# Optimization experiments

Hardware: AMD Instinct MI355X
Metric: run time of the kernel (lower is better)

The kernel has to match this reference:

```python
import jax, jax.numpy as jnp
import numpy as np

BATCH = 256
NUM_PIXELS = 4096
NUM_LATENT = 8192
NUM_STEPS = 50
STEP_SIZE = 0.1
SPARSE_MULT = 0.1
EPS = 1e-8


def setup_inputs() -> dict:
    key = jax.random.key(0)
    k1, k2 = jax.random.split(key)
    input_tensor = jax.random.normal(k1, (BATCH, NUM_PIXELS), dtype=jnp.float32)
    w = jax.random.normal(k2, (NUM_PIXELS, NUM_LATENT), dtype=jnp.float32)
    # l2-normalize each dictionary element (column over pixel dim), as in dp.l2_normalize_weights
    w = w / (jnp.linalg.norm(w, axis=0, keepdims=True) + EPS)
    return {"input_tensor": input_tensor, "w": w}


def _threshold(u):
    # soft threshold with rectify_a=True: a = max(u - lambda, 0)
    return jnp.where(u > SPARSE_MULT, u - SPARSE_MULT, jnp.zeros_like(u))


def reference(input_tensor, w):
    # excitatory drive b = x @ w, constant over inference steps  [B, L]
    excitatory = jnp.matmul(input_tensor, w)
    # inhibitory Gram matrix G = w^T w - I  [L, L]
    gram = jnp.matmul(w.T, w) - jnp.eye(NUM_LATENT, dtype=w.dtype)

    def body(u, _):
        a = _threshold(u)
        du = excitatory - jnp.matmul(a, gram) - u
        return u + STEP_SIZE * du, None

    u0 = jnp.zeros((input_tensor.shape[0], NUM_LATENT), dtype=input_tensor.dtype)
    u_final, _ = jax.lax.scan(body, u0, None, length=NUM_STEPS - 1)
    a_final = _threshold(u_final)
    # reconstruction = a @ w^T  [B, P]
    return jnp.matmul(a_final, w.T)
```

## Files before the change

kernel.cpp:

```cpp
#include <hip/hip_runtime.h>
#include <stdint.h>
#include <math.h>

#define B_DIM 256
#define P_DIM 4096
#define L_DIM 8192
#define NSTEPS 50
#define STEP 0.1f
#define LAM 0.1f
#define FP8_ITERS 42
#define GSCALE 64.0f
#define ASCALE 16.0f
#define INV_SCALE (1.0f / (64.0f * 16.0f))

typedef __attribute__((ext_vector_type(8))) short bf16x8;
typedef __attribute__((ext_vector_type(4))) float f32x4;
typedef __attribute__((ext_vector_type(4))) int i32x4;
typedef __attribute__((ext_vector_type(8))) int i32x8;

__device__ __forceinline__ unsigned short f2bf(float f) {
    union { float f; uint32_t u; } x; x.f = f;
    uint32_t r = (x.u + 0x7FFF + ((x.u >> 16) & 1)) >> 16;
    return (unsigned short)r;
}
__device__ __forceinline__ float bf2f(unsigned short h) {
    union { uint32_t u; float f; } x; x.u = (uint32_t)h << 16; return x.f;
}


__global__ void cast_x_kernel(const float* __restrict__ in, unsigned short* __restrict__ out, int n) {
    int i = (blockIdx.x * blockDim.x + threadIdx.x) * 4;
    if (i < n) {
        float4 v = *(const float4*)&in[i];
        ushort4 o;
        o.x = f2bf(v.x); o.y = f2bf(v.y); o.z = f2bf(v.z); o.w = f2bf(v.w);
        *(ushort4*)&out[i] = o;
    }
}

__global__ void cast_transpose_w(const float* __restrict__ w,
                                 unsigned short* __restrict__ w_bf,
                                 unsigned short* __restrict__ wT_bf) {
    __shared__ float tile[32][33];
    int c0 = blockIdx.x * 32;
    int r0 = blockIdx.y * 32;
    int tx = threadIdx.x, ty = threadIdx.y;
#pragma unroll
    for (int i = ty; i < 32; i += 8) {
        float v = w[(size_t)(r0 + i) * L_DIM + c0 + tx];
        tile[i][tx] = v;
        w_bf[(size_t)(r0 + i) * L_DIM + c0 + tx] = f2bf(v);
    }
    __syncthreads();
#pragma unroll
    for (int i = ty; i < 32; i += 8) {
        wT_bf[(size_t)(c0 + i) * P_DIM + r0 + tx] = f2bf(tile[tx][i]);
    }
}

__global__ void quantize_G(const unsigned short* __restrict__ G, unsigned char* __restrict__ Gf) {
    size_t i = ((size_t)blockIdx.x * 256 + threadIdx.x) * 8;
    bf16x8 v = *(const bf16x8*)&G[i];
    float f[8];
#pragma unroll
    for (int j = 0; j < 8; ++j) f[j] = bf2f((unsigned short)v[j]) * GSCALE;
    int q0 = __builtin_amdgcn_cvt_pk_fp8_f32(f[0], f[1], 0, false);
    q0 = __builtin_amdgcn_cvt_pk_fp8_f32(f[2], f[3], q0, true);
    int q1 = __builtin_amdgcn_cvt_pk_fp8_f32(f[4], f[5], 0, false);
    q1 = __builtin_amdgcn_cvt_pk_fp8_f32(f[6], f[7], q1, true);
    const int r = (int)(i & 127);
    size_t dst = (i & ~(size_t)127) + (size_t)((((r >> 6) & 1) << 6) + (((r >> 3) & 3) << 4) + (((r >> 5) & 1) << 3));
    *(int2*)(Gf + dst) = make_int2(q0, q1);
}

template <int BM, int BN, int BK, int WMC, int WNC, int EPI, int MM, int NN, int KK, int MAP>
__global__ __launch_bounds__(WMC * WNC * 64)
void gemm_pipe(const unsigned short* __restrict__ A,
               const unsigned short* __restrict__ Bt,
               float* __restrict__ Cf,
               float* __restrict__ uvec,
               unsigned short* __restrict__ aout,
               unsigned char* __restrict__ afp8) {
    constexpr int NWAVES = WMC * WNC;
    constexpr int WM = BM / WMC, WN = BN / WNC;
    constexpr int MF = WM / 16, NF = WN / 16;
    constexpr int ACH = BM / (8 * NWAVES);
    constexpr int BCH = BN / (8 * NWAVES);
    constexpr int LPS = ACH + BCH;
    constexpr int NT = KK / BK;
    static_assert(BK == 64, "swizzle hardcoded for BK=64");
    static_assert(ACH * 8 * NWAVES == BM && BCH * 8 * NWAVES == BN, "stage geometry");
    static_assert(NT % 4 == 0 && NT >= 8, "pipeline geometry");

    __shared__ __align__(16) unsigned short As[4][BM * BK];
    __shared__ __align__(16) unsigned short Bs[4][BN * BK];

    const int tid = threadIdx.x;
    const int w = tid >> 6;
    const int l = tid & 63;
    const int wr = w / WNC, wc = w % WNC;

    const int id = blockIdx.x;
    int bx, by;
    if constexpr (MAP == 0) {
        constexpr int PPX = (NN / BN) / 8;
        static_assert(MM / BM == 4 && (NN / BN) % 8 == 0, "panel map geometry");
        bx = (id & 7) * PPX + ((id >> 3) >> 2);
        by = (id >> 3) & 3;
    } else {
        constexpr int GY = MM / BM;
        by = id % GY;
        bx = id / GY;
    }
    const int row0 = by * BM;
    const int col0 = bx * BN;

    const int lrow = l >> 3;
    const int lcol = (((l & 7) ^ lrow) * 8);

    const unsigned short* gA = A + (size_t)(row0 + lrow) * KK + lcol;
    const unsigned short* gB = Bt + (size_t)(col0 + lrow) * KK + lcol;

    auto stage = [&](int buf, int k0) {
#pragma unroll
        for (int i = 0; i < ACH; ++i) {
            const int chunk = i * NWAVES + w;
            __builtin_amdgcn_global_load_lds(
                (const __attribute__((address_space(1))) void*)(gA + (size_t)chunk * 8 * KK + k0),
                (__attribute__((address_space(3))) void*)(&As[buf][chunk * 512]), 16, 0, 0);
        }
#pragma unroll
        for (int i = 0; i < BCH; ++i) {
            const int chunk = i * NWAVES + w;
            __builtin_amdgcn_global_load_lds(
                (const __attribute__((address_space(1))) void*)(gB + (size_t)chunk * 8 * KK + k0),
                (__attribute__((address_space(3))) void*)(&Bs[buf][chunk * 512]), 16, 0, 0);
        }
    };

    f32x4 acc[MF][NF] = {};

    auto compute = [&](int buf) {
#pragma unroll
        for (int kk = 0; kk < BK; kk += 32) {
            const int kslot = (kk >> 3) + (l >> 4);
            bf16x8 af[MF], bfr[NF];
#pragma unroll
            for (int mf = 0; mf < MF; ++mf) {
                const int arow = wr * WM + mf * 16 + (l & 15);
                af[mf] = *(const bf16x8*)&As[buf][arow * BK + ((kslot ^ (arow & 7)) << 3)];
            }
#pragma unroll
            for (int nf = 0; nf < NF; ++nf) {
                const int brow = wc * WN + nf * 16 + (l & 15);
                bfr[nf] = *(const bf16x8*)&Bs[buf][brow * BK + ((kslot ^ (brow & 7)) << 3)];
            }
#pragma unroll
            for (int mf = 0; mf < MF; ++mf)
#pragma unroll
                for (int nf = 0; nf < NF; ++nf)
                    acc[mf][nf] = __builtin_amdgcn_mfma_f32_16x16x32_bf16(
                        af[mf], bfr[nf], acc[mf][nf], 0, 0, 0);
        }
    };

#define PH(BUF, TT, WAITN, DOSTG)                                            \
    asm volatile("s_waitcnt vmcnt(%0)" ::"i"(WAITN) : "memory");             \
    __builtin_amdgcn_s_barrier();                                            \
    asm volatile("" ::: "memory");                                           \
    if (DOSTG) stage((BUF + 3) & 3, ((TT) + 3) * BK);                        \
    compute(BUF);

    stage(0, 0);
    stage(1, BK);
    stage(2, 2 * BK);
#pragma unroll 1
    for (int t = 0; t < NT - 4; t += 4) {
        PH(0, t + 0, 2 * LPS, true)
        PH(1, t + 1, 2 * LPS, true)
        PH(2, t + 2, 2 * LPS, true)
        PH(3, t + 3, 2 * LPS, true)
    }
    PH(0, NT - 4, 2 * LPS, true)
    PH(1, NT - 3, 2 * LPS, false)
    PH(2, NT - 2, LPS, false)
    PH(3, NT - 1, 0, false)
#undef PH

    const int er = (l >> 4) * 4;
    const int ec = l & 15;
#pragma unroll
    for (int mf = 0; mf < MF; ++mf) {
#pragma unroll
        for (int nf = 0; nf < NF; ++nf) {
#pragma unroll
            for (int j = 0; j < 4; ++j) {
                int gr = row0 + wr * WM + mf * 16 + er + j;
                int gc = col0 + wc * WN + nf * 16 + ec;
                size_t idx = (size_t)gr * NN + gc;
                float v = acc[mf][nf][j];
                if constexpr (EPI == 1) {
                    Cf[idx] = v;
                    float u0 = STEP * v;
                    uvec[idx] = u0;
                    float a = (u0 > LAM) ? (u0 - LAM) : 0.0f;
                    aout[idx] = f2bf(a);
                    float a16 = a * ASCALE;
                    int q = __builtin_amdgcn_cvt_pk_fp8_f32(a16, a16, 0, false);
                    const int r = gc & 127;
                    size_t fd = (size_t)gr * L_DIM + (size_t)(gc & ~127) +
                                (size_t)((((r >> 6) & 1) << 6) + (((r >> 3) & 3) << 4) + (((r >> 5) & 1) << 3) + (r & 7));
                    afp8[fd] = (unsigned char)(q & 0xff);
                } else {
                    Cf[idx] = v;
                }
            }
        }
    }
}

__global__ __launch_bounds__(512, 2)
void gemm_gram_sym(const unsigned short* __restrict__ A,
                   unsigned short* __restrict__ G) {
    constexpr int BM = 256, BN = 256, BK = 64;
    constexpr int WMC = 2, WNC = 4, NWAVES = 8;
    constexpr int WM = 128, WN = 64, MF = 8, NF = 4;
    constexpr int ACH = 4, BCH = 4, LPS = 8;
    constexpr int NT = P_DIM / BK;

    __shared__ __align__(16) unsigned short sh[4 * 256 * 64];
#define ASB(buf) (sh + (buf) * (256 * 64))
#define BSB(buf) (sh + (2 + (buf)) * (256 * 64))

    const int tid = threadIdx.x;
    const int w = tid >> 6;
    const int l = tid & 63;
    const int wr = w / WNC, wc = w % WNC;

    const int id = blockIdx.x;
    const int i = (int)((65.0f - sqrtf(4225.0f - 8.0f * (float)id)) * 0.5f);
    const int cum = i * (65 - i) / 2;
    const int j = i + (id - cum);
    const int by = i, bx = j;
    const int row0 = by * BM;
    const int col0 = bx * BN;

    const int lrow = l >> 3;
    const int lcol = (((l & 7) ^ lrow) * 8);

    const unsigned short* gA = A + (size_t)(row0 + lrow) * P_DIM + lcol;
    const unsigned short* gB = A + (size_t)(col0 + lrow) * P_DIM + lcol;

    auto stage = [&](int buf, int t) {
        const int k0 = t * BK;
#pragma unroll
        for (int c = 0; c < ACH; ++c) {
            const int chunk = c * NWAVES + w;
            __builtin_amdgcn_global_load_lds(
                (const __attribute__((address_space(1))) void*)(gA + (size_t)chunk * 8 * P_DIM + k0),
                (__attribute__((address_space(3))) void*)(ASB(buf) + chunk * 512), 16, 0, 0);
        }
#pragma unroll
        for (int c = 0; c < BCH; ++c) {
            const int chunk = c * NWAVES + w;
            __builtin_amdgcn_global_load_lds(
                (const __attribute__((address_space(1))) void*)(gB + (size_t)chunk * 8 * P_DIM + k0),
                (__attribute__((address_space(3))) void*)(BSB(buf) + chunk * 512), 16, 0, 0);
        }
    };

    f32x4 acc[MF][NF] = {};

    auto compute = [&](int buf) {
#pragma unroll
        for (int kk = 0; kk < BK; kk += 32) {
            const int kslot = (kk >> 3) + (l >> 4);
            bf16x8 af[MF], bfr[NF];
#pragma unroll
            for (int mf = 0; mf < MF; ++mf) {
                const int arow = wr * WM + mf * 16 + (l & 15);
                af[mf] = *(const bf16x8*)&ASB(buf)[arow * BK + ((kslot ^ (arow & 7)) << 3)];
            }
#pragma unroll
            for (int nf = 0; nf < NF; ++nf) {
                const int brow = wc * WN + nf * 16 + (l & 15);
                bfr[nf] = *(const bf16x8*)&BSB(buf)[brow * BK + ((kslot ^ (brow & 7)) << 3)];
            }
#pragma unroll
            for (int mf = 0; mf < MF; ++mf)
#pragma unroll
                for (int nf = 0; nf < NF; ++nf)
                    acc[mf][nf] = __builtin_amdgcn_mfma_f32_16x16x32_bf16(
                        af[mf], bfr[nf], acc[mf][nf], 0, 0, 0);
        }
    };

#define PH2(BUF, WAITN, DOSTG, TT)                                           \
    asm volatile("s_waitcnt vmcnt(%0)" ::"i"(WAITN) : "memory");             \
    __builtin_amdgcn_s_barrier();                                            \
    asm volatile("" ::: "memory");                                           \
    compute(BUF);                                                            \
    __builtin_amdgcn_s_barrier();                                            \
    asm volatile("" ::: "memory");                                           \
    if (DOSTG) stage(BUF, (TT) + 2);

    stage(0, 0);
    stage(1, 1);
#pragma unroll 1
    for (int t = 0; t < NT - 2; t += 2) {
        PH2(0, LPS, true, t)
        PH2(1, LPS, true, t + 1)
    }
    PH2(0, LPS, false, 0)
    PH2(1, 0, false, 0)
#undef PH2

    const int er = (l >> 4) * 4;
    const int ec = l & 15;

#pragma unroll
    for (int mf = 0; mf < MF; ++mf)
#pragma unroll
        for (int nf = 0; nf < NF; ++nf)
#pragma unroll
            for (int jj = 0; jj < 4; ++jj) {
                int gr = row0 + wr * WM + mf * 16 + er + jj;
                int gc = col0 + wc * WN + nf * 16 + ec;
                float v = acc[mf][nf][jj];
                if (gr == gc) v -= 1.0f;
                G[(size_t)gr * L_DIM + gc] = f2bf(v);
            }

    if (by != bx) {
        unsigned short* T = sh;
#pragma unroll 1
        for (int p = 0; p < 2; ++p) {
            __syncthreads();
            if ((wc >> 1) == p) {
#pragma unroll
                for (int mf = 0; mf < MF; ++mf)
#pragma unroll
                    for (int nf = 0; nf < NF; ++nf)
#pragma unroll
                        for (int jj = 0; jj < 4; ++jj) {
                            const int gr_l = wr * WM + mf * 16 + er + jj;
                            const int gc_l = (wc & 1) * 64 + nf * 16 + ec;
                            T[gc_l * 256 + (gr_l ^ ((gc_l & 7) << 2))] = f2bf(acc[mf][nf][jj]);
                        }
            }
            __syncthreads();
            const int rr = tid >> 6;
            const int cc = (tid & 63) * 4;
#pragma unroll
            for (int s = 0; s < 16; ++s) {
                const int r = s * 8 + rr;
                uint2 val = *(const uint2*)&T[r * 256 + (cc ^ ((r & 7) << 2))];
                *(uint2*)&G[(size_t)(col0 + p * 128 + r) * L_DIM + row0 + cc] = val;
            }
        }
    }
#undef ASB
#undef BSB
}

template <int BM, int BN, int WMC, int WNC, int EPI, int KROW, int KLOOP, int MAP>
__global__ __launch_bounds__(WMC * WNC * 64, 2)
void gemm2(const unsigned short* __restrict__ A,
           const unsigned short* __restrict__ Bt,
           unsigned short* __restrict__ Obf) {
    constexpr int NWAVES = WMC * WNC;
    constexpr int WM = BM / WMC, WN = BN / WNC;
    constexpr int MF = WM / 16, NF = WN / 16;
    constexpr int ACH = BM / (8 * NWAVES);
    constexpr int BCH = BN / (8 * NWAVES);
    constexpr int LPS = ACH + BCH;
    constexpr int BK = 64;
    constexpr int NT = KLOOP / BK;
    static_assert(ACH * 8 * NWAVES == BM && BCH * 8 * NWAVES == BN, "stage geometry");
    static_assert(NT % 2 == 0 && NT >= 4, "pipeline geometry");

    __shared__ __align__(16) unsigned short As[2][BM * BK];
    __shared__ __align__(16) unsigned short Bs[2][BN * BK];

    const int tid = threadIdx.x;
    const int w = tid >> 6;
    const int l = tid & 63;
    const int wr = w / WNC, wc = w % WNC;

    const int id = blockIdx.x;
    int bx, by, koff;
    size_t o_off;
    {
        const int xcd = id & 7;
        by = (id >> 3) & 1;
        const int pp = id >> 4;
        const int slice = pp & 3;
        bx = xcd * 4 + (pp >> 2);
        koff = slice * KLOOP;
        o_off = (size_t)slice * B_DIM * L_DIM;
    }
    const int row0 = by * BM;
    const int col0 = bx * BN;

    const int lrow = l >> 3;
    const int lcol = (((l & 7) ^ lrow) * 8);

    const unsigned short* gA = A + (size_t)(row0 + lrow) * KROW + koff + lcol;
    const unsigned short* gB = Bt + (size_t)(col0 + lrow) * KROW + koff + lcol;

    auto stage = [&](int buf, int t) {
        const int k0 = t * BK;
#pragma unroll
        for (int i = 0; i < ACH; ++i) {
            const int chunk = i * NWAVES + w;
            __builtin_amdgcn_global_load_lds(
                (const __attribute__((address_space(1))) void*)(gA + (size_t)chunk * 8 * KROW + k0),
                (__attribute__((address_space(3))) void*)(&As[buf][chunk * 512]), 16, 0, 0);
        }
#pragma unroll
        for (int i = 0; i < BCH; ++i) {
            const int chunk = i * NWAVES + w;
            __builtin_amdgcn_global_load_lds(
                (const __attribute__((address_space(1))) void*)(gB + (size_t)chunk * 8 * KROW + k0),
                (__attribute__((address_space(3))) void*)(&Bs[buf][chunk * 512]), 16, 0, 0);
        }
    };

    f32x4 acc[MF][NF] = {};

    auto compute = [&](int buf) {
#pragma unroll
        for (int kk = 0; kk < BK; kk += 32) {
            const int kslot = (kk >> 3) + (l >> 4);
            bf16x8 af[MF], bfr[NF];
#pragma unroll
            for (int mf = 0; mf < MF; ++mf) {
                const int arow = wr * WM + mf * 16 + (l & 15);
                af[mf] = *(const bf16x8*)&As[buf][arow * BK + ((kslot ^ (arow & 7)) << 3)];
            }
#pragma unroll
            for (int nf = 0; nf < NF; ++nf) {
                const int brow = wc * WN + nf * 16 + (l & 15);
                bfr[nf] = *(const bf16x8*)&Bs[buf][brow * BK + ((kslot ^ (brow & 7)) << 3)];
            }
#pragma unroll
            for (int mf = 0; mf < MF; ++mf)
#pragma unroll
                for (int nf = 0; nf < NF; ++nf)
                    acc[mf][nf] = __builtin_amdgcn_mfma_f32_16x16x32_bf16(
                        af[mf], bfr[nf], acc[mf][nf], 0, 0, 0);
        }
    };

#define PH2(BUF, WAITN, DOSTG, TT)                                           \
    asm volatile("s_waitcnt vmcnt(%0)" ::"i"(WAITN) : "memory");             \
    __builtin_amdgcn_s_barrier();                                            \
    asm volatile("" ::: "memory");                                           \
    compute(BUF);                                                            \
    __builtin_amdgcn_s_barrier();                                            \
    asm volatile("" ::: "memory");                                           \
    if (DOSTG) stage(BUF, (TT) + 2);

    stage(0, 0);
    stage(1, 1);
#pragma unroll 1
    for (int t = 0; t < NT - 2; t += 2) {
        PH2(0, LPS, true, t)
        PH2(1, LPS, true, t + 1)
    }
    PH2(0, LPS, false, 0)
    PH2(1, 0, false, 0)
#undef PH2

    const int er = (l >> 4) * 4;
    const int ec = l & 15;
#pragma unroll
    for (int mf = 0; mf < MF; ++mf)
#pragma unroll
        for (int nf = 0; nf < NF; ++nf)
#pragma unroll
            for (int j = 0; j < 4; ++j) {
                int gr = row0 + wr * WM + mf * 16 + er + j;
                int gc = col0 + wc * WN + nf * 16 + ec;
                Obf[o_off + (size_t)gr * L_DIM + gc] = f2bf(acc[mf][nf][j]);
            }
}

template <int BM, int BN, int WMC, int WNC>
__global__ __launch_bounds__(WMC * WNC * 64, 2)
void gemm_fp8(const unsigned char* __restrict__ A,
              const unsigned char* __restrict__ Bt,
              unsigned short* __restrict__ Obf) {
    constexpr int NWAVES = WMC * WNC;
    constexpr int WM = BM / WMC, WN = BN / WNC;
    constexpr int MF = WM / 16, NF = WN / 16;
    constexpr int BKB = 128;
    constexpr int ACH = BM / (8 * NWAVES);
    constexpr int BCH = BN / (8 * NWAVES);
    constexpr int LPS = ACH + BCH;
    constexpr int KLOOP = 2048;
    constexpr int NT = KLOOP / BKB;
    constexpr int KKB = L_DIM;
    static_assert(ACH * 8 * NWAVES == BM && BCH * 8 * NWAVES == BN, "stage geometry");

    __shared__ __align__(16) unsigned char As[2][BM * BKB];
    __shared__ __align__(16) unsigned char Bs[2][BN * BKB];

    const int tid = threadIdx.x;
    const int w = tid >> 6;
    const int l = tid & 63;
    const int wr = w / WNC, wc = w % WNC;

    const int id = blockIdx.x;
    const int xcd = id & 7;
    const int by = (id >> 3) & 1;
    const int pp = id >> 4;
    const int slice = pp & 3;
    const int bx = xcd * 4 + (pp >> 2);
    const int row0 = by * BM;
    const int col0 = bx * BN;
    const int koff = slice * KLOOP;

    const int lrow = l >> 3;
    const int lcol = (((l & 7) ^ lrow) << 4);

    const unsigned char* gA = A + (size_t)(row0 + lrow) * KKB + koff + lcol;
    const unsigned char* gB = Bt + (size_t)(col0 + lrow) * KKB + koff + lcol;

    auto stage = [&](int buf, int t) {
        const int k0 = t * BKB;
#pragma unroll
        for (int i = 0; i < ACH; ++i) {
            const int chunk = i * NWAVES + w;
            __builtin_amdgcn_global_load_lds(
                (const __attribute__((address_space(1))) void*)(gA + (size_t)chunk * 8 * KKB + k0),
                (__attribute__((address_space(3))) void*)(&As[buf][chunk * 1024]), 16, 0, 0);
        }
#pragma unroll
        for (int i = 0; i < BCH; ++i) {
            const int chunk = i * NWAVES + w;
            __builtin_amdgcn_global_load_lds(
                (const __attribute__((address_space(1))) void*)(gB + (size_t)chunk * 8 * KKB + k0),
                (__attribute__((address_space(3))) void*)(&Bs[buf][chunk * 1024]), 16, 0, 0);
        }
    };

    f32x4 acc[MF][NF] = {};

    auto compute = [&](int buf) {
        const int g = l >> 4;
        i32x8 a8[MF], b8[NF];
#pragma unroll
        for (int mf = 0; mf < MF; ++mf) {
            const int arow = wr * WM + mf * 16 + (l & 15);
            i32x4 lo = *(const i32x4*)&As[buf][arow * BKB + (((g) ^ (arow & 7)) << 4)];
            i32x4 hi = *(const i32x4*)&As[buf][arow * BKB + (((4 + g) ^ (arow & 7)) << 4)];
            a8[mf] = i32x8{lo[0], lo[1], lo[2], lo[3], hi[0], hi[1], hi[2], hi[3]};
        }
#pragma unroll
        for (int nf = 0; nf < NF; ++nf) {
            const int brow = wc * WN + nf * 16 + (l & 15);
            i32x4 lo = *(const i32x4*)&Bs[buf][brow * BKB + (((g) ^ (brow & 7)) << 4)];
            i32x4 hi = *(const i32x4*)&Bs[buf][brow * BKB + (((4 + g) ^ (brow & 7)) << 4)];
            b8[nf] = i32x8{lo[0], lo[1], lo[2], lo[3], hi[0], hi[1], hi[2], hi[3]};
        }
#pragma unroll
        for (int mf = 0; mf < MF; ++mf)
#pragma unroll
            for (int nf = 0; nf < NF; ++nf)
                acc[mf][nf] = __builtin_amdgcn_mfma_scale_f32_16x16x128_f8f6f4(
                    a8[mf], b8[nf], acc[mf][nf],
                    0, 0,
                    0, 127,
                    0, 127);
    };

#define PH2(BUF, WAITN, DOSTG, TT)                                           \
    asm volatile("s_waitcnt vmcnt(%0)" ::"i"(WAITN) : "memory");             \
    __builtin_amdgcn_s_barrier();                                            \
    asm volatile("" ::: "memory");                                           \
    compute(BUF);                                                            \
    __builtin_amdgcn_s_barrier();                                            \
    asm volatile("" ::: "memory");                                           \
    if (DOSTG) stage(BUF, (TT) + 2);

    stage(0, 0);
    stage(1, 1);
#pragma unroll 1
    for (int t = 0; t < NT - 2; t += 2) {
        PH2(0, LPS, true, t)
        PH2(1, LPS, true, t + 1)
    }
    PH2(0, LPS, false, 0)
    PH2(1, 0, false, 0)
#undef PH2

    const int er = (l >> 4) * 4;
    const int ec = l & 15;
    const size_t o_off = (size_t)slice * B_DIM * L_DIM;
#pragma unroll
    for (int mf = 0; mf < MF; ++mf)
#pragma unroll
        for (int nf = 0; nf < NF; ++nf)
#pragma unroll
            for (int j = 0; j < 4; ++j) {
                int gr = row0 + wr * WM + mf * 16 + er + j;
                int gc = col0 + wc * WN + nf * 16 + ec;
                Obf[o_off + (size_t)gr * L_DIM + gc] = f2bf(acc[mf][nf][j] * INV_SCALE);
            }
}

__global__ void reduce_iter(const unsigned short* __restrict__ P,
                            const float* __restrict__ bv,
                            float* __restrict__ uv,
                            unsigned short* __restrict__ an,
                            unsigned char* __restrict__ anf) {
    constexpr size_t SL = (size_t)B_DIM * L_DIM;
    size_t i = ((size_t)blockIdx.x * 256 + threadIdx.x) * 8;
    float s[8] = {};
#pragma unroll
    for (int sl = 0; sl < 4; ++sl) {
        ushort4 p0 = *(const ushort4*)&P[sl * SL + i];
        ushort4 p1 = *(const ushort4*)&P[sl * SL + i + 4];
        s[0] += bf2f(p0.x); s[1] += bf2f(p0.y); s[2] += bf2f(p0.z); s[3] += bf2f(p0.w);
        s[4] += bf2f(p1.x); s[5] += bf2f(p1.y); s[6] += bf2f(p1.z); s[7] += bf2f(p1.w);
    }
    float4 b0 = *(const float4*)&bv[i];
    float4 b1 = *(const float4*)&bv[i + 4];
    float4 u0 = *(const float4*)&uv[i];
    float4 u1 = *(const float4*)&uv[i + 4];
    float un[8];
    un[0] = 0.9f * u0.x + STEP * b0.x - STEP * s[0];
    un[1] = 0.9f * u0.y + STEP * b0.y - STEP * s[1];
    un[2] = 0.9f * u0.z + STEP * b0.z - STEP * s[2];
    un[3] = 0.9f * u0.w + STEP * b0.w - STEP * s[3];
    un[4] = 0.9f * u1.x + STEP * b1.x - STEP * s[4];
    un[5] = 0.9f * u1.y + STEP * b1.y - STEP * s[5];
    un[6] = 0.9f * u1.z + STEP * b1.z - STEP * s[6];
    un[7] = 0.9f * u1.w + STEP * b1.w - STEP * s[7];
    *(float4*)&uv[i] = make_float4(un[0], un[1], un[2], un[3]);
    *(float4*)&uv[i + 4] = make_float4(un[4], un[5], un[6], un[7]);
    float a[8];
#pragma unroll
    for (int j = 0; j < 8; ++j) a[j] = (un[j] > LAM) ? (un[j] - LAM) : 0.0f;
    ushort4 o0, o1;
    o0.x = f2bf(a[0]); o0.y = f2bf(a[1]); o0.z = f2bf(a[2]); o0.w = f2bf(a[3]);
    o1.x = f2bf(a[4]); o1.y = f2bf(a[5]); o1.z = f2bf(a[6]); o1.w = f2bf(a[7]);
    *(ushort4*)&an[i] = o0;
    *(ushort4*)&an[i + 4] = o1;
    int q0 = __builtin_amdgcn_cvt_pk_fp8_f32(a[0] * ASCALE, a[1] * ASCALE, 0, false);
    q0 = __builtin_amdgcn_cvt_pk_fp8_f32(a[2] * ASCALE, a[3] * ASCALE, q0, true);
    int q1 = __builtin_amdgcn_cvt_pk_fp8_f32(a[4] * ASCALE, a[5] * ASCALE, 0, false);
    q1 = __builtin_amdgcn_cvt_pk_fp8_f32(a[6] * ASCALE, a[7] * ASCALE, q1, true);
    const int r = (int)(i & 127);
    size_t dst = (i & ~(size_t)127) + (size_t)((((r >> 6) & 1) << 6) + (((r >> 3) & 3) << 4) + (((r >> 5) & 1) << 3));
    *(int2*)(anf + dst) = make_int2(q0, q1);
}

extern "C" void kernel_launch(void* const* d_in, const int* in_sizes, int n_in,
                              void* d_out, int out_size, void* d_ws, size_t ws_size,
                              hipStream_t stream) {
    (void)in_sizes; (void)n_in; (void)out_size; (void)ws_size;
    const float* x = (const float*)d_in[0];
    const float* w = (const float*)d_in[1];
    float* out = (float*)d_out;

    char* ws = (char*)d_ws;
    unsigned short* wT  = (unsigned short*)ws;
    unsigned char*  Gf  = (unsigned char*)ws;
    unsigned short* wbf = wT + (size_t)L_DIM * P_DIM;
    unsigned short* G   = wbf + (size_t)P_DIM * L_DIM;
    float* bv = (float*)(G + (size_t)L_DIM * L_DIM);
    float* uv = bv + (size_t)B_DIM * L_DIM;
    unsigned short* a0 = (unsigned short*)(uv + (size_t)B_DIM * L_DIM);
    unsigned short* a1 = a0 + (size_t)B_DIM * L_DIM;
    unsigned short* xbf = a1 + (size_t)B_DIM * L_DIM;
    unsigned char* a0f = (unsigned char*)(xbf + (size_t)B_DIM * P_DIM);
    unsigned char* a1f = a0f + (size_t)B_DIM * L_DIM;
    unsigned short* Ppart = (unsigned short*)(a1f + (size_t)B_DIM * L_DIM);

    cast_x_kernel<<<(B_DIM * P_DIM / 4 + 255) / 256, 256, 0, stream>>>(x, xbf, B_DIM * P_DIM);
    cast_transpose_w<<<dim3(L_DIM / 32, P_DIM / 32), dim3(32, 8), 0, stream>>>(w, wbf, wT);

    gemm_gram_sym<<<528, 512, 0, stream>>>(wT, G);

    gemm_pipe<64, 128, 64, 2, 4, 1, B_DIM, L_DIM, P_DIM, 0><<<256, 512, 0, stream>>>(
        xbf, wT, bv, uv, a0, a0f);

    quantize_G<<<(int)(((size_t)L_DIM * L_DIM / 8) / 256), 256, 0, stream>>>(G, Gf);

    unsigned short* ac = a0; unsigned short* an = a1;
    unsigned char* acf = a0f; unsigned char* anf = a1f;
    for (int it = 0; it < FP8_ITERS; ++it) {
        gemm_fp8<128, 256, 2, 4><<<256, 512, 0, stream>>>(acf, Gf, Ppart);
        reduce_iter<<<(B_DIM * L_DIM) / (256 * 8), 256, 0, stream>>>(Ppart, bv, uv, an, anf);
        unsigned short* t = ac; ac = an; an = t;
        unsigned char* tf = acf; acf = anf; anf = tf;
    }
    for (int it = 0; it < (NSTEPS - 2) - FP8_ITERS; ++it) {
        gemm2<128, 256, 2, 4, 4, L_DIM, 2048, 3><<<256, 512, 0, stream>>>(ac, G, Ppart);
        reduce_iter<<<(B_DIM * L_DIM) / (256 * 8), 256, 0, stream>>>(Ppart, bv, uv, an, anf);
        unsigned short* t = ac; ac = an; an = t;
        unsigned char* tf = acf; acf = anf; anf = tf;
    }

    gemm_pipe<64, 64, 64, 2, 4, 3, B_DIM, P_DIM, L_DIM, 0><<<256, 512, 0, stream>>>(
        ac, wbf, out, nullptr, nullptr, nullptr);
}
```

Before: 2.064 ms.

## Use full-batch 256x256 FP8 tiles with 8-way split-K and matching reduce

The FP8 Gram GEMM now uses one 256x256 tile covering the whole batch instead of 128x256 tiles split over two row blocks. The K split goes from 4 slices of 2048 to 8 slices of 1024. Each G tile is therefore streamed once rather than twice, which cuts global/L2 traffic for the large G matrix. The A fragments are loaded per row inside the MFMA loop to hold down register pressure, and occupancy drops to one block per CU. A new reduce kernel sums 8 bf16 partials instead of 4, which doubles partial-sum write and read traffic in the reduce step.

```diff
diff --git a/kernel.cpp b/kernel.cpp
--- a/kernel.cpp
+++ b/kernel.cpp
@@ -486,22 +486,21 @@
             }
 }
 
-template <int BM, int BN, int WMC, int WNC>
-__global__ __launch_bounds__(WMC * WNC * 64, 2)
+__global__ __launch_bounds__(512, 1)
 void gemm_fp8(const unsigned char* __restrict__ A,
               const unsigned char* __restrict__ Bt,
               unsigned short* __restrict__ Obf) {
-    constexpr int NWAVES = WMC * WNC;
-    constexpr int WM = BM / WMC, WN = BN / WNC;
-    constexpr int MF = WM / 16, NF = WN / 16;
+    constexpr int NWAVES = 8;
+    constexpr int BM = 256, BN = 256;
+    constexpr int WMC = 2, WNC = 4;
+    constexpr int WM = 128, WN = 64, MF = 8, NF = 4;
     constexpr int BKB = 128;
     constexpr int ACH = BM / (8 * NWAVES);
     constexpr int BCH = BN / (8 * NWAVES);
     constexpr int LPS = ACH + BCH;
-    constexpr int KLOOP = 2048;
+    constexpr int KLOOP = 1024;
     constexpr int NT = KLOOP / BKB;
     constexpr int KKB = L_DIM;
-    static_assert(ACH * 8 * NWAVES == BM && BCH * 8 * NWAVES == BN, "stage geometry");
 
     __shared__ __align__(16) unsigned char As[2][BM * BKB];
     __shared__ __align__(16) unsigned char Bs[2][BN * BKB];
@@ -513,18 +512,16 @@
 
     const int id = blockIdx.x;
     const int xcd = id & 7;
-    const int by = (id >> 3) & 1;
-    const int pp = id >> 4;
-    const int slice = pp & 3;
-    const int bx = xcd * 4 + (pp >> 2);
-    const int row0 = by * BM;
+    const int q = id >> 3;
+    const int slice = q & 7;
+    const int bx = xcd * 4 + (q >> 3);
     const int col0 = bx * BN;
     const int koff = slice * KLOOP;
 
     const int lrow = l >> 3;
     const int lcol = (((l & 7) ^ lrow) << 4);
 
-    const unsigned char* gA = A + (size_t)(row0 + lrow) * KKB + koff + lcol;
+    const unsigned char* gA = A + (size_t)lrow * KKB + koff + lcol;
     const unsigned char* gB = Bt + (size_t)(col0 + lrow) * KKB + koff + lcol;
 
     auto stage = [&](int buf, int t) {
@@ -549,14 +546,7 @@
 
     auto compute = [&](int buf) {
         const int g = l >> 4;
-        i32x8 a8[MF], b8[NF];
-#pragma unroll
-        for (int mf = 0; mf < MF; ++mf) {
-            const int arow = wr * WM + mf * 16 + (l & 15);
-            i32x4 lo = *(const i32x4*)&As[buf][arow * BKB + (((g) ^ (arow & 7)) << 4)];
-            i32x4 hi = *(const i32x4*)&As[buf][arow * BKB + (((4 + g) ^ (arow & 7)) << 4)];
-            a8[mf] = i32x8{lo[0], lo[1], lo[2], lo[3], hi[0], hi[1], hi[2], hi[3]};
-        }
+        i32x8 b8[NF];
 #pragma unroll
         for (int nf = 0; nf < NF; ++nf) {
             const int brow = wc * WN + nf * 16 + (l & 15);
@@ -565,14 +555,19 @@
             b8[nf] = i32x8{lo[0], lo[1], lo[2], lo[3], hi[0], hi[1], hi[2], hi[3]};
         }
 #pragma unroll
-        for (int mf = 0; mf < MF; ++mf)
+        for (int mf = 0; mf < MF; ++mf) {
+            const int arow = wr * WM + mf * 16 + (l & 15);
+            i32x4 lo = *(const i32x4*)&As[buf][arow * BKB + (((g) ^ (arow & 7)) << 4)];
+            i32x4 hi = *(const i32x4*)&As[buf][arow * BKB + (((4 + g) ^ (arow & 7)) << 4)];
+            i32x8 a8 = i32x8{lo[0], lo[1], lo[2], lo[3], hi[0], hi[1], hi[2], hi[3]};
 #pragma unroll
             for (int nf = 0; nf < NF; ++nf)
                 acc[mf][nf] = __builtin_amdgcn_mfma_scale_f32_16x16x128_f8f6f4(
-                    a8[mf], b8[nf], acc[mf][nf],
+                    a8, b8[nf], acc[mf][nf],
                     0, 0,
                     0, 127,
                     0, 127);
+        }
     };
 
 #define PH2(BUF, WAITN, DOSTG, TT)                                           \
@@ -604,17 +599,17 @@
         for (int nf = 0; nf < NF; ++nf)
 #pragma unroll
             for (int j = 0; j < 4; ++j) {
-                int gr = row0 + wr * WM + mf * 16 + er + j;
+                int gr = wr * WM + mf * 16 + er + j;
                 int gc = col0 + wc * WN + nf * 16 + ec;
                 Obf[o_off + (size_t)gr * L_DIM + gc] = f2bf(acc[mf][nf][j] * INV_SCALE);
             }
 }
 
-__global__ void reduce_iter(const unsigned short* __restrict__ P,
-                            const float* __restrict__ bv,
-                            float* __restrict__ uv,
-                            unsigned short* __restrict__ an,
-                            unsigned char* __restrict__ anf) {
+__global__ void reduce_iter4(const unsigned short* __restrict__ P,
+                             const float* __restrict__ bv,
+                             float* __restrict__ uv,
+                             unsigned short* __restrict__ an,
+                             unsigned char* __restrict__ anf) {
     constexpr size_t SL = (size_t)B_DIM * L_DIM;
     size_t i = ((size_t)blockIdx.x * 256 + threadIdx.x) * 8;
     float s[8] = {};
@@ -657,6 +652,53 @@
     *(int2*)(anf + dst) = make_int2(q0, q1);
 }
 
+__global__ void reduce_iter8(const unsigned short* __restrict__ P,
+                             const float* __restrict__ bv,
+                             float* __restrict__ uv,
+                             unsigned short* __restrict__ an,
+                             unsigned char* __restrict__ anf) {
+    constexpr size_t SL = (size_t)B_DIM * L_DIM;
+    size_t i = ((size_t)blockIdx.x * 256 + threadIdx.x) * 8;
+    float s[8] = {};
+#pragma unroll
+    for (int sl = 0; sl < 8; ++sl) {
+        ushort4 p0 = *(const ushort4*)&P[sl * SL + i];
+        ushort4 p1 = *(const ushort4*)&P[sl * SL + i + 4];
+        s[0] += bf2f(p0.x); s[1] += bf2f(p0.y); s[2] += bf2f(p0.z); s[3] += bf2f(p0.w);
+        s[4] += bf2f(p1.x); s[5] += bf2f(p1.y); s[6] += bf2f(p1.z); s[7] += bf2f(p1.w);
+    }
+    float4 b0 = *(const float4*)&bv[i];
+    float4 b1 = *(const float4*)&bv[i + 4];
+    float4 u0 = *(const float4*)&uv[i];
+    float4 u1 = *(const float4*)&uv[i + 4];
+    float un[8];
+    un[0] = 0.9f * u0.x + STEP * b0.x - STEP * s[0];
+    un[1] = 0.9f * u0.y + STEP * b0.y - STEP * s[1];
+    un[2] = 0.9f * u0.z + STEP * b0.z - STEP * s[2];
+    un[3] = 0.9f * u0.w + STEP * b0.w - STEP * s[3];
+    un[4] = 0.9f * u1.x + STEP * b1.x - STEP * s[4];
+    un[5] = 0.9f * u1.y + STEP * b1.y - STEP * s[5];
+    un[6] = 0.9f * u1.z + STEP * b1.z - STEP * s[6];
+    un[7] = 0.9f * u1.w + STEP * b1.w - STEP * s[7];
+    *(float4*)&uv[i] = make_float4(un[0], un[1], un[2], un[3]);
+    *(float4*)&uv[i + 4] = make_float4(un[4], un[5], un[6], un[7]);
+    float a[8];
+#pragma unroll
+    for (int j = 0; j < 8; ++j) a[j] = (un[j] > LAM) ? (un[j] - LAM) : 0.0f;
+    ushort4 o0, o1;
+    o0.x = f2bf(a[0]); o0.y = f2bf(a[1]); o0.z = f2bf(a[2]); o0.w = f2bf(a[3]);
+    o1.x = f2bf(a[4]); o1.y = f2bf(a[5]); o1.z = f2bf(a[6]); o1.w = f2bf(a[7]);
+    *(ushort4*)&an[i] = o0;
+    *(ushort4*)&an[i + 4] = o1;
+    int q0 = __builtin_amdgcn_cvt_pk_fp8_f32(a[0] * ASCALE, a[1] * ASCALE, 0, false);
+    q0 = __builtin_amdgcn_cvt_pk_fp8_f32(a[2] * ASCALE, a[3] * ASCALE, q0, true);
+    int q1 = __builtin_amdgcn_cvt_pk_fp8_f32(a[4] * ASCALE, a[5] * ASCALE, 0, false);
+    q1 = __builtin_amdgcn_cvt_pk_fp8_f32(a[6] * ASCALE, a[7] * ASCALE, q1, true);
+    const int r = (int)(i & 127);
+    size_t dst = (i & ~(size_t)127) + (size_t)((((r >> 6) & 1) << 6) + (((r >> 3) & 3) << 4) + (((r >> 5) & 1) << 3));
+    *(int2*)(anf + dst) = make_int2(q0, q1);
+}
+
 extern "C" void kernel_launch(void* const* d_in, const int* in_sizes, int n_in,
                               void* d_out, int out_size, void* d_ws, size_t ws_size,
                               hipStream_t stream) {
@@ -692,14 +734,14 @@
     unsigned short* ac = a0; unsigned short* an = a1;
     unsigned char* acf = a0f; unsigned char* anf = a1f;
     for (int it = 0; it < FP8_ITERS; ++it) {
-        gemm_fp8<128, 256, 2, 4><<<256, 512, 0, stream>>>(acf, Gf, Ppart);
-        reduce_iter<<<(B_DIM * L_DIM) / (256 * 8), 256, 0, stream>>>(Ppart, bv, uv, an, anf);
+        gemm_fp8<<<256, 512, 0, stream>>>(acf, Gf, Ppart);
+        reduce_iter8<<<(B_DIM * L_DIM) / (256 * 8), 256, 0, stream>>>(Ppart, bv, uv, an, anf);
         unsigned short* t = ac; ac = an; an = t;
         unsigned char* tf = acf; acf = anf; anf = tf;
     }
     for (int it = 0; it < (NSTEPS - 2) - FP8_ITERS; ++it) {
         gemm2<128, 256, 2, 4, 4, L_DIM, 2048, 3><<<256, 512, 0, stream>>>(ac, G, Ppart);
-        reduce_iter<<<(B_DIM * L_DIM) / (256 * 8), 256, 0, stream>>>(Ppart, bv, uv, an, anf);
+        reduce_iter4<<<(B_DIM * L_DIM) / (256 * 8), 256, 0, stream>>>(Ppart, bv, uv, an, anf);
         unsigned short* t = ac; ac = an; an = t;
         unsigned char* tf = acf; acf = anf; anf = tf;
     }
```

Measured after the change: 2.346 ms. 1.14x slower.
